# Kernel tuning notes

Measured on AMD Instinct MI355X. Metric: run time of the kernel, lower is better.

## Reference

```python
import jax, jax.numpy as jnp
import numpy as np

# 8 neighbor offsets (dy, dx) matching the torch module's kernel order:
# TL, T, TR, L, R, BL, B, BR
OFFSETS = [(-1, -1), (-1, 0), (-1, 1), (0, -1), (0, 1), (1, -1), (1, 0), (1, 1)]


def _cos_map(x):
    # x: [B, C, H, W] -> [B, 8, H-2, W-2]
    B, C, H, W = x.shape
    c = x[:, :, 1:H - 1, 1:W - 1]                       # center pixels
    xx = jnp.sum(c * c, axis=1, keepdims=True)          # [B,1,H-2,W-2]
    rxx = jax.lax.rsqrt(xx)
    maps = []
    for dy, dx in OFFSETS:
        n = x[:, :, 1 + dy:H - 1 + dy, 1 + dx:W - 1 + dx]  # shifted neighbor
        dot = jnp.sum(c * n, axis=1, keepdims=True)
        aa = jnp.sum(n * n, axis=1, keepdims=True)
        # ((x+a)^2 sum - (x^2+a^2) sum)/2 == dot; then cosine scaling
        maps.append(dot * rxx * jax.lax.rsqrt(aa))
    return jnp.concatenate(maps, axis=1)                # [B,8,H-2,W-2]


def setup_inputs() -> dict:
    key = jax.random.key(0)
    k1, k2 = jax.random.split(key)
    B, C, H, W = 16, 19, 256, 256
    preds = jax.random.normal(k1, (B, C, H, W), dtype=jnp.float32)
    soft = jax.random.normal(k2, (B, C, H, W), dtype=jnp.float32)
    return {"preds": preds, "soft": soft}


def reference(preds, soft):
    graph_s = _cos_map(preds)
    graph_t = _cos_map(soft)
    return jnp.mean((graph_s - graph_t) ** 2)
```

## Files before the change

kernel.cpp:

```cpp
#include <hip/hip_runtime.h>
#include <math.h>


constexpr int BATCH = 16;
constexpr int CH = 19;
constexpr int H = 256;
constexpr int W = 256;

constexpr int TX = 64;
constexpr int TY = 8;
constexpr int TW = TX + 2;
constexpr int THH = TY + 2;
constexpr int TILE = TW * THH;
constexpr int NTHREADS = TX * TY;

__global__ __launch_bounds__(NTHREADS)
void cosmap_mse_kernel(const float* __restrict__ preds,
                       const float* __restrict__ soft,
                       double* __restrict__ acc) {
  __shared__ float sp[TILE];
  __shared__ float ss[TILE];
  __shared__ float rnp[TILE];
  __shared__ float rns[TILE];

  const int tx = threadIdx.x;
  const int ty = threadIdx.y;
  const int tid = ty * TX + tx;
  const int b = blockIdx.z;
  const int x0 = 1 + blockIdx.x * TX;
  const int y0 = 1 + blockIdx.y * TY;

  const int idx0 = tid;
  const bool has2 = (tid + NTHREADS) < TILE;
  const int idx1 = has2 ? tid + NTHREADS : tid;

  auto goff = [&](int idx) -> int {
    int j = idx / TW;
    int i = idx - j * TW;
    int gy = y0 - 1 + j; gy = gy > H - 1 ? H - 1 : gy;
    int gx = x0 - 1 + i; gx = gx > W - 1 ? W - 1 : gx;
    return gy * W + gx;
  };
  const int off0 = goff(idx0);
  const int off1 = goff(idx1);

  const size_t base = (size_t)b * CH * H * W;
  const float* pp = preds + base;
  const float* ps = soft + base;

  float dotp[8], dots[8];
#pragma unroll
  for (int k = 0; k < 8; ++k) { dotp[k] = 0.f; dots[k] = 0.f; }
  float xxp0 = 0.f, xxs0 = 0.f, xxp1 = 0.f, xxs1 = 0.f;

  const int ci = (ty + 1) * TW + (tx + 1);

  for (int c = 0; c < CH; ++c) {
    const size_t cb = (size_t)c * (H * W);
    float vp0 = pp[cb + off0];
    float vs0 = ps[cb + off0];
    float vp1 = pp[cb + off1];
    float vs1 = ps[cb + off1];
    sp[idx0] = vp0; ss[idx0] = vs0;
    if (has2) { sp[idx1] = vp1; ss[idx1] = vs1; }
    xxp0 = fmaf(vp0, vp0, xxp0); xxs0 = fmaf(vs0, vs0, xxs0);
    xxp1 = fmaf(vp1, vp1, xxp1); xxs1 = fmaf(vs1, vs1, xxs1);
    __syncthreads();

    const float cp = sp[ci];
    const float cs = ss[ci];
    constexpr int offs[8] = {-TW - 1, -TW, -TW + 1, -1, 1, TW - 1, TW, TW + 1};
#pragma unroll
    for (int k = 0; k < 8; ++k) {
      dotp[k] = fmaf(cp, sp[ci + offs[k]], dotp[k]);
      dots[k] = fmaf(cs, ss[ci + offs[k]], dots[k]);
    }
    __syncthreads();
  }

  rnp[idx0] = 1.0f / sqrtf(xxp0);
  rns[idx0] = 1.0f / sqrtf(xxs0);
  if (has2) {
    rnp[idx1] = 1.0f / sqrtf(xxp1);
    rns[idx1] = 1.0f / sqrtf(xxs1);
  }
  __syncthreads();

  float local = 0.f;
  const int px = x0 + tx;
  const int py = y0 + ty;
  if (px < W - 1 && py < H - 1) {
    const float rp = rnp[ci];
    const float rs = rns[ci];
    constexpr int offs[8] = {-TW - 1, -TW, -TW + 1, -1, 1, TW - 1, TW, TW + 1};
#pragma unroll
    for (int k = 0; k < 8; ++k) {
      float mp = dotp[k] * rp * rnp[ci + offs[k]];
      float ms = dots[k] * rs * rns[ci + offs[k]];
      float d = mp - ms;
      local = fmaf(d, d, local);
    }
  }

#pragma unroll
  for (int o = 32; o > 0; o >>= 1) local += __shfl_down(local, o, 64);
  __shared__ float wsum[NTHREADS / 64];
  const int wid = tid >> 6;
  const int lane = tid & 63;
  if (lane == 0) wsum[wid] = local;
  __syncthreads();
  if (tid == 0) {
    float s = 0.f;
#pragma unroll
    for (int w = 0; w < NTHREADS / 64; ++w) s += wsum[w];
    atomicAdd(acc, (double)s);
  }
}

__global__ void finalize_kernel(const double* __restrict__ acc,
                                float* __restrict__ out) {
  constexpr double cnt = (double)BATCH * 8.0 * (H - 2) * (W - 2);
  out[0] = (float)(acc[0] / cnt);
}

extern "C" void kernel_launch(void* const* d_in, const int* in_sizes, int n_in,
                              void* d_out, int out_size, void* d_ws, size_t ws_size,
                              hipStream_t stream) {
  const float* preds = (const float*)d_in[0];
  const float* soft = (const float*)d_in[1];
  double* acc = (double*)d_ws;

  hipMemsetAsync(d_ws, 0, sizeof(double), stream);

  dim3 block(TX, TY);
  dim3 grid((W - 2 + TX - 1) / TX, (H - 2 + TY - 1) / TY, BATCH);
  cosmap_mse_kernel<<<grid, block, 0, stream>>>(preds, soft, acc);
  finalize_kernel<<<1, 1, 0, stream>>>(acc, (float*)d_out);
}
```

Measured before the change: 199.4 us.

## Compute two pixels per thread with float2 loads and double-buffered shared tiles

Each thread now handles two horizontally adjacent output pixels, using float2 global loads and float2 shared-memory tiles 128 pixels wide. Shared tiles are double-buffered per channel, so only one barrier per channel is needed, and the next channel's global loads are issued before the barrier as a software prefetch. The goal is fewer load instructions, fewer barriers and better reuse of neighbour values across the two pixels. In exchange it uses more registers, launches half as many blocks, and needs extra edge handling for the right border column.

Result: faster. 183.5 us (-8.0%).

```diff
diff --git a/kernel.cpp b/kernel.cpp
--- a/kernel.cpp
+++ b/kernel.cpp
@@ -2,118 +2,161 @@
 #include <math.h>
 
 
-constexpr int BATCH = 16;
-constexpr int CH = 19;
-constexpr int H = 256;
-constexpr int W = 256;
+constexpr int BATCH = 16, CH = 19, H = 256, W = 256;
+constexpr int BXT = 64, BYT = 8, NT = BXT * BYT;
+constexpr int CX = 128, CY = 8;
+constexpr int TW2 = 66;
+constexpr int TH = 10;
+constexpr int NP = TW2 * TH;
 
-constexpr int TX = 64;
-constexpr int TY = 8;
-constexpr int TW = TX + 2;
-constexpr int THH = TY + 2;
-constexpr int TILE = TW * THH;
-constexpr int NTHREADS = TX * TY;
-
-__global__ __launch_bounds__(NTHREADS)
+__global__ __launch_bounds__(NT)
 void cosmap_mse_kernel(const float* __restrict__ preds,
                        const float* __restrict__ soft,
-                       double* __restrict__ acc) {
-  __shared__ float sp[TILE];
-  __shared__ float ss[TILE];
-  __shared__ float rnp[TILE];
-  __shared__ float rns[TILE];
+                       double* __restrict__ acc_out) {
+  __shared__ float2 sp[2][NP];
+  __shared__ float2 ss[2][NP];
+  __shared__ float wsum[NT / 64];
 
-  const int tx = threadIdx.x;
-  const int ty = threadIdx.y;
-  const int tid = ty * TX + tx;
-  const int b = blockIdx.z;
-  const int x0 = 1 + blockIdx.x * TX;
-  const int y0 = 1 + blockIdx.y * TY;
+  const int tx = threadIdx.x, ty = threadIdx.y;
+  const int tid = ty * BXT + tx;
+  const int x0 = 1 + blockIdx.x * CX;
+  const int y0 = 1 + blockIdx.y * CY;
 
-  const int idx0 = tid;
-  const bool has2 = (tid + NTHREADS) < TILE;
-  const int idx1 = has2 ? tid + NTHREADS : tid;
+  const int p0 = tid;
+  const bool has2 = tid < (NP - NT);
+  const int p1 = has2 ? tid + NT : tid;
 
-  auto goff = [&](int idx) -> int {
-    int j = idx / TW;
-    int i = idx - j * TW;
+  bool ov0 = false, ov1 = false;
+  int e0, e1;
+  {
+    int j = p0 / TW2, i2 = p0 - j * TW2;
     int gy = y0 - 1 + j; gy = gy > H - 1 ? H - 1 : gy;
-    int gx = x0 - 1 + i; gx = gx > W - 1 ? W - 1 : gx;
-    return gy * W + gx;
-  };
-  const int off0 = goff(idx0);
-  const int off1 = goff(idx1);
+    int gs = x0 - 1 + 2 * i2;
+    ov0 = gs >= W - 1;
+    e0 = gy * W + (ov0 ? W - 2 : gs);
+  }
+  {
+    int j = p1 / TW2, i2 = p1 - j * TW2;
+    int gy = y0 - 1 + j; gy = gy > H - 1 ? H - 1 : gy;
+    int gs = x0 - 1 + 2 * i2;
+    ov1 = gs >= W - 1;
+    e1 = gy * W + (ov1 ? W - 2 : gs);
+  }
 
-  const size_t base = (size_t)b * CH * H * W;
-  const float* pp = preds + base;
-  const float* ps = soft + base;
+  const size_t base = (size_t)blockIdx.z * CH * H * W;
+  const float2* pp = (const float2*)(preds + base);
+  const float2* qq = (const float2*)(soft + base);
+  const int f0 = e0 >> 1, f1 = e1 >> 1;
+  constexpr int CS2 = H * W / 2;
 
-  float dotp[8], dots[8];
+  float2 vp0 = pp[f0], vq0 = qq[f0], vp1 = pp[f1], vq1 = qq[f1];
+
+  float a[8], bb[8], c[8], d[8];
 #pragma unroll
-  for (int k = 0; k < 8; ++k) { dotp[k] = 0.f; dots[k] = 0.f; }
-  float xxp0 = 0.f, xxs0 = 0.f, xxp1 = 0.f, xxs1 = 0.f;
+  for (int k = 0; k < 8; ++k) { a[k] = 0.f; bb[k] = 0.f; c[k] = 0.f; d[k] = 0.f; }
+  float2 np0 = {0.f, 0.f}, np1 = {0.f, 0.f}, nq0 = {0.f, 0.f}, nq1 = {0.f, 0.f};
 
-  const int ci = (ty + 1) * TW + (tx + 1);
+  const int r0 = ty * TW2 + tx;
 
-  for (int c = 0; c < CH; ++c) {
-    const size_t cb = (size_t)c * (H * W);
-    float vp0 = pp[cb + off0];
-    float vs0 = ps[cb + off0];
-    float vp1 = pp[cb + off1];
-    float vs1 = ps[cb + off1];
-    sp[idx0] = vp0; ss[idx0] = vs0;
-    if (has2) { sp[idx1] = vp1; ss[idx1] = vs1; }
-    xxp0 = fmaf(vp0, vp0, xxp0); xxs0 = fmaf(vs0, vs0, xxs0);
-    xxp1 = fmaf(vp1, vp1, xxp1); xxs1 = fmaf(vs1, vs1, xxs1);
-    __syncthreads();
-
-    const float cp = sp[ci];
-    const float cs = ss[ci];
-    constexpr int offs[8] = {-TW - 1, -TW, -TW + 1, -1, 1, TW - 1, TW, TW + 1};
-#pragma unroll
-    for (int k = 0; k < 8; ++k) {
-      dotp[k] = fmaf(cp, sp[ci + offs[k]], dotp[k]);
-      dots[k] = fmaf(cs, ss[ci + offs[k]], dots[k]);
+  for (int ch = 0; ch < CH; ++ch) {
+    float2* SP = sp[ch & 1];
+    float2* SS = ss[ch & 1];
+    float2 wp0 = vp0; if (ov0) wp0.x = wp0.y;
+    float2 wq0 = vq0; if (ov0) wq0.x = wq0.y;
+    float2 wp1 = vp1; if (ov1) wp1.x = wp1.y;
+    float2 wq1 = vq1; if (ov1) wq1.x = wq1.y;
+    SP[p0] = wp0; SS[p0] = wq0;
+    if (has2) { SP[p1] = wp1; SS[p1] = wq1; }
+    np0.x = fmaf(wp0.x, wp0.x, np0.x); np0.y = fmaf(wp0.y, wp0.y, np0.y);
+    nq0.x = fmaf(wq0.x, wq0.x, nq0.x); nq0.y = fmaf(wq0.y, wq0.y, nq0.y);
+    if (has2) {
+      np1.x = fmaf(wp1.x, wp1.x, np1.x); np1.y = fmaf(wp1.y, wp1.y, np1.y);
+      nq1.x = fmaf(wq1.x, wq1.x, nq1.x); nq1.y = fmaf(wq1.y, wq1.y, nq1.y);
+    }
+    if (ch + 1 < CH) {
+      const int o = (ch + 1) * CS2;
+      vp0 = pp[f0 + o]; vq0 = qq[f0 + o];
+      vp1 = pp[f1 + o]; vq1 = qq[f1 + o];
     }
     __syncthreads();
+    {
+      float2 u0 = SP[r0],           u1 = SP[r0 + 1];
+      float2 m0 = SP[r0 + TW2],     m1 = SP[r0 + TW2 + 1];
+      float2 l0 = SP[r0 + 2 * TW2], l1 = SP[r0 + 2 * TW2 + 1];
+      float c0 = m0.y, c1 = m1.x;
+      a[0] = fmaf(c0, u0.x, a[0]); a[1] = fmaf(c0, u0.y, a[1]); a[2] = fmaf(c0, u1.x, a[2]);
+      a[3] = fmaf(c0, m0.x, a[3]); a[4] = fmaf(c0, m1.x, a[4]);
+      a[5] = fmaf(c0, l0.x, a[5]); a[6] = fmaf(c0, l0.y, a[6]); a[7] = fmaf(c0, l1.x, a[7]);
+      bb[0] = fmaf(c1, u0.y, bb[0]); bb[1] = fmaf(c1, u1.x, bb[1]); bb[2] = fmaf(c1, u1.y, bb[2]);
+      bb[3] = fmaf(c1, m0.y, bb[3]); bb[4] = fmaf(c1, m1.y, bb[4]);
+      bb[5] = fmaf(c1, l0.y, bb[5]); bb[6] = fmaf(c1, l1.x, bb[6]); bb[7] = fmaf(c1, l1.y, bb[7]);
+    }
+    {
+      float2 u0 = SS[r0],           u1 = SS[r0 + 1];
+      float2 m0 = SS[r0 + TW2],     m1 = SS[r0 + TW2 + 1];
+      float2 l0 = SS[r0 + 2 * TW2], l1 = SS[r0 + 2 * TW2 + 1];
+      float c0 = m0.y, c1 = m1.x;
+      c[0] = fmaf(c0, u0.x, c[0]); c[1] = fmaf(c0, u0.y, c[1]); c[2] = fmaf(c0, u1.x, c[2]);
+      c[3] = fmaf(c0, m0.x, c[3]); c[4] = fmaf(c0, m1.x, c[4]);
+      c[5] = fmaf(c0, l0.x, c[5]); c[6] = fmaf(c0, l0.y, c[6]); c[7] = fmaf(c0, l1.x, c[7]);
+      d[0] = fmaf(c1, u0.y, d[0]); d[1] = fmaf(c1, u1.x, d[1]); d[2] = fmaf(c1, u1.y, d[2]);
+      d[3] = fmaf(c1, m0.y, d[3]); d[4] = fmaf(c1, m1.y, d[4]);
+      d[5] = fmaf(c1, l0.y, d[5]); d[6] = fmaf(c1, l1.x, d[6]); d[7] = fmaf(c1, l1.y, d[7]);
+    }
   }
 
-  rnp[idx0] = 1.0f / sqrtf(xxp0);
-  rns[idx0] = 1.0f / sqrtf(xxs0);
-  if (has2) {
-    rnp[idx1] = 1.0f / sqrtf(xxp1);
-    rns[idx1] = 1.0f / sqrtf(xxs1);
+  {
+    float2 r;
+    r.x = 1.0f / sqrtf(np0.x); r.y = 1.0f / sqrtf(np0.y); sp[1][p0] = r;
+    r.x = 1.0f / sqrtf(nq0.x); r.y = 1.0f / sqrtf(nq0.y); ss[1][p0] = r;
+    if (has2) {
+      r.x = 1.0f / sqrtf(np1.x); r.y = 1.0f / sqrtf(np1.y); sp[1][p1] = r;
+      r.x = 1.0f / sqrtf(nq1.x); r.y = 1.0f / sqrtf(nq1.y); ss[1][p1] = r;
+    }
   }
   __syncthreads();
 
   float local = 0.f;
-  const int px = x0 + tx;
-  const int py = y0 + ty;
-  if (px < W - 1 && py < H - 1) {
-    const float rp = rnp[ci];
-    const float rs = rns[ci];
-    constexpr int offs[8] = {-TW - 1, -TW, -TW + 1, -1, 1, TW - 1, TW, TW + 1};
+  {
+    const float2* RP = sp[1];
+    const float2* RS = ss[1];
+    float2 u0 = RP[r0],           u1 = RP[r0 + 1];
+    float2 m0 = RP[r0 + TW2],     m1 = RP[r0 + TW2 + 1];
+    float2 l0 = RP[r0 + 2 * TW2], l1 = RP[r0 + 2 * TW2 + 1];
+    float2 su0 = RS[r0],           su1 = RS[r0 + 1];
+    float2 sm0 = RS[r0 + TW2],     sm1 = RS[r0 + TW2 + 1];
+    float2 sl0 = RS[r0 + 2 * TW2], sl1 = RS[r0 + 2 * TW2 + 1];
+    float rc0 = m0.y, rc1 = m1.x, sc0 = sm0.y, sc1 = sm1.x;
+    float n0p[8] = {u0.x, u0.y, u1.x, m0.x, m1.x, l0.x, l0.y, l1.x};
+    float n1p[8] = {u0.y, u1.x, u1.y, m0.y, m1.y, l0.y, l1.x, l1.y};
+    float n0s[8] = {su0.x, su0.y, su1.x, sm0.x, sm1.x, sl0.x, sl0.y, sl1.x};
+    float n1s[8] = {su0.y, su1.x, su1.y, sm0.y, sm1.y, sl0.y, sl1.x, sl1.y};
+    float acc0 = 0.f, acc1 = 0.f;
 #pragma unroll
     for (int k = 0; k < 8; ++k) {
-      float mp = dotp[k] * rp * rnp[ci + offs[k]];
-      float ms = dots[k] * rs * rns[ci + offs[k]];
-      float d = mp - ms;
-      local = fmaf(d, d, local);
+      float mp = a[k] * rc0 * n0p[k];
+      float ms = c[k] * sc0 * n0s[k];
+      float dd = mp - ms;
+      acc0 = fmaf(dd, dd, acc0);
+      float mp1 = bb[k] * rc1 * n1p[k];
+      float ms1 = d[k] * sc1 * n1s[k];
+      float d1v = mp1 - ms1;
+      acc1 = fmaf(d1v, d1v, acc1);
     }
+    const int cgx = x0 + 2 * tx, cgy = y0 + ty;
+    const bool vy = cgy <= H - 2;
+    local = (vy && cgx <= W - 2 ? acc0 : 0.f) + (vy && cgx + 1 <= W - 2 ? acc1 : 0.f);
   }
 
 #pragma unroll
   for (int o = 32; o > 0; o >>= 1) local += __shfl_down(local, o, 64);
-  __shared__ float wsum[NTHREADS / 64];
-  const int wid = tid >> 6;
-  const int lane = tid & 63;
-  if (lane == 0) wsum[wid] = local;
+  if ((tid & 63) == 0) wsum[tid >> 6] = local;
   __syncthreads();
   if (tid == 0) {
     float s = 0.f;
 #pragma unroll
-    for (int w = 0; w < NTHREADS / 64; ++w) s += wsum[w];
-    atomicAdd(acc, (double)s);
+    for (int w = 0; w < NT / 64; ++w) s += wsum[w];
+    atomicAdd(acc_out, (double)s);
   }
 }
 
@@ -132,8 +175,8 @@
 
   hipMemsetAsync(d_ws, 0, sizeof(double), stream);
 
-  dim3 block(TX, TY);
-  dim3 grid((W - 2 + TX - 1) / TX, (H - 2 + TY - 1) / TY, BATCH);
+  dim3 block(BXT, BYT);
+  dim3 grid((W - 2 + CX - 1) / CX, (H - 2 + CY - 1) / CY, BATCH);
   cosmap_mse_kernel<<<grid, block, 0, stream>>>(preds, soft, acc);
   finalize_kernel<<<1, 1, 0, stream>>>(acc, (float*)d_out);
 }
```

## Replace shared-memory tiles with per-wave row processing using float4 loads and shuffles

Applied to the files above, without the earlier changes.

Each wavefront now handles one output row across the full width. Every lane loads float4 vectors from the three adjacent rows for both inputs and exchanges horizontal neighbors with lane shuffles instead of shared memory and block barriers. The next channel's loads are prefetched in registers, and each wave issues its own atomic add. This removes LDS traffic and __syncthreads, but each input row is now read three times (once per neighboring output row), and register pressure goes up.

Result: slower. 210.2 us (+5.4%).

```diff
diff --git a/kernel.cpp b/kernel.cpp
--- a/kernel.cpp
+++ b/kernel.cpp
@@ -2,119 +2,111 @@
 #include <math.h>
 
 
-constexpr int BATCH = 16;
-constexpr int CH = 19;
-constexpr int H = 256;
-constexpr int W = 256;
+constexpr int BATCH = 16, CH = 19, H = 256, W = 256;
+constexpr int HW = H * W;
+constexpr int CS4 = HW / 4;
 
-constexpr int TX = 64;
-constexpr int TY = 8;
-constexpr int TW = TX + 2;
-constexpr int THH = TY + 2;
-constexpr int TILE = TW * THH;
-constexpr int NTHREADS = TX * TY;
-
-__global__ __launch_bounds__(NTHREADS)
+__global__ __launch_bounds__(256)
 void cosmap_mse_kernel(const float* __restrict__ preds,
                        const float* __restrict__ soft,
-                       double* __restrict__ acc) {
-  __shared__ float sp[TILE];
-  __shared__ float ss[TILE];
-  __shared__ float rnp[TILE];
-  __shared__ float rns[TILE];
+                       double* __restrict__ acc_out) {
+  const int lane = threadIdx.x & 63;
+  const int wid = threadIdx.x >> 6;
+  const int y = 1 + (blockIdx.y << 2) + wid;
+  if (y > H - 2) return;
+  const size_t base = (size_t)blockIdx.z * (CH * HW);
 
-  const int tx = threadIdx.x;
-  const int ty = threadIdx.y;
-  const int tid = ty * TX + tx;
-  const int b = blockIdx.z;
-  const int x0 = 1 + blockIdx.x * TX;
-  const int y0 = 1 + blockIdx.y * TY;
+  const float4* PU = (const float4*)(preds + base + (size_t)(y - 1) * W) + lane;
+  const float4* PM = PU + (W / 4);
+  const float4* PL = PM + (W / 4);
+  const float4* SU = (const float4*)(soft + base + (size_t)(y - 1) * W) + lane;
+  const float4* SM = SU + (W / 4);
+  const float4* SL = SM + (W / 4);
 
-  const int idx0 = tid;
-  const bool has2 = (tid + NTHREADS) < TILE;
-  const int idx1 = has2 ? tid + NTHREADS : tid;
+  float dp[8][4], dq[8][4];
+  float np[3][4], nq[3][4];
+#pragma unroll
+  for (int d = 0; d < 8; ++d)
+#pragma unroll
+    for (int e = 0; e < 4; ++e) { dp[d][e] = 0.f; dq[d][e] = 0.f; }
+#pragma unroll
+  for (int r = 0; r < 3; ++r)
+#pragma unroll
+    for (int e = 0; e < 4; ++e) { np[r][e] = 0.f; nq[r][e] = 0.f; }
 
-  auto goff = [&](int idx) -> int {
-    int j = idx / TW;
-    int i = idx - j * TW;
-    int gy = y0 - 1 + j; gy = gy > H - 1 ? H - 1 : gy;
-    int gx = x0 - 1 + i; gx = gx > W - 1 ? W - 1 : gx;
-    return gy * W + gx;
-  };
-  const int off0 = goff(idx0);
-  const int off1 = goff(idx1);
-
-  const size_t base = (size_t)b * CH * H * W;
-  const float* pp = preds + base;
-  const float* ps = soft + base;
-
-  float dotp[8], dots[8];
-#pragma unroll
-  for (int k = 0; k < 8; ++k) { dotp[k] = 0.f; dots[k] = 0.f; }
-  float xxp0 = 0.f, xxs0 = 0.f, xxp1 = 0.f, xxs1 = 0.f;
-
-  const int ci = (ty + 1) * TW + (tx + 1);
+  float4 au = PU[0], am = PM[0], al = PL[0];
+  float4 bu = SU[0], bm = SM[0], bl = SL[0];
 
   for (int c = 0; c < CH; ++c) {
-    const size_t cb = (size_t)c * (H * W);
-    float vp0 = pp[cb + off0];
-    float vs0 = ps[cb + off0];
-    float vp1 = pp[cb + off1];
-    float vs1 = ps[cb + off1];
-    sp[idx0] = vp0; ss[idx0] = vs0;
-    if (has2) { sp[idx1] = vp1; ss[idx1] = vs1; }
-    xxp0 = fmaf(vp0, vp0, xxp0); xxs0 = fmaf(vs0, vs0, xxs0);
-    xxp1 = fmaf(vp1, vp1, xxp1); xxs1 = fmaf(vs1, vs1, xxs1);
-    __syncthreads();
-
-    const float cp = sp[ci];
-    const float cs = ss[ci];
-    constexpr int offs[8] = {-TW - 1, -TW, -TW + 1, -1, 1, TW - 1, TW, TW + 1};
+    const float4 cu = au, cm = am, cl = al, eu = bu, em = bm, el = bl;
+    if (c + 1 < CH) {
+      const int o = (c + 1) * CS4;
+      au = PU[o]; am = PM[o]; al = PL[o];
+      bu = SU[o]; bm = SM[o]; bl = SL[o];
+    }
+    const float wu[6] = {__shfl_up(cu.w, 1), cu.x, cu.y, cu.z, cu.w, __shfl_down(cu.x, 1)};
+    const float wm[6] = {__shfl_up(cm.w, 1), cm.x, cm.y, cm.z, cm.w, __shfl_down(cm.x, 1)};
+    const float wl[6] = {__shfl_up(cl.w, 1), cl.x, cl.y, cl.z, cl.w, __shfl_down(cl.x, 1)};
+    const float vu[6] = {__shfl_up(eu.w, 1), eu.x, eu.y, eu.z, eu.w, __shfl_down(eu.x, 1)};
+    const float vm[6] = {__shfl_up(em.w, 1), em.x, em.y, em.z, em.w, __shfl_down(em.x, 1)};
+    const float vl[6] = {__shfl_up(el.w, 1), el.x, el.y, el.z, el.w, __shfl_down(el.x, 1)};
 #pragma unroll
-    for (int k = 0; k < 8; ++k) {
-      dotp[k] = fmaf(cp, sp[ci + offs[k]], dotp[k]);
-      dots[k] = fmaf(cs, ss[ci + offs[k]], dots[k]);
+    for (int e = 0; e < 4; ++e) {
+      np[0][e] = fmaf(wu[e + 1], wu[e + 1], np[0][e]);
+      np[1][e] = fmaf(wm[e + 1], wm[e + 1], np[1][e]);
+      np[2][e] = fmaf(wl[e + 1], wl[e + 1], np[2][e]);
+      nq[0][e] = fmaf(vu[e + 1], vu[e + 1], nq[0][e]);
+      nq[1][e] = fmaf(vm[e + 1], vm[e + 1], nq[1][e]);
+      nq[2][e] = fmaf(vl[e + 1], vl[e + 1], nq[2][e]);
+      const float cp = wm[e + 1], cs = vm[e + 1];
+      dp[0][e] = fmaf(cp, wu[e],     dp[0][e]); dq[0][e] = fmaf(cs, vu[e],     dq[0][e]);
+      dp[1][e] = fmaf(cp, wu[e + 1], dp[1][e]); dq[1][e] = fmaf(cs, vu[e + 1], dq[1][e]);
+      dp[2][e] = fmaf(cp, wu[e + 2], dp[2][e]); dq[2][e] = fmaf(cs, vu[e + 2], dq[2][e]);
+      dp[3][e] = fmaf(cp, wm[e],     dp[3][e]); dq[3][e] = fmaf(cs, vm[e],     dq[3][e]);
+      dp[4][e] = fmaf(cp, wm[e + 2], dp[4][e]); dq[4][e] = fmaf(cs, vm[e + 2], dq[4][e]);
+      dp[5][e] = fmaf(cp, wl[e],     dp[5][e]); dq[5][e] = fmaf(cs, vl[e],     dq[5][e]);
+      dp[6][e] = fmaf(cp, wl[e + 1], dp[6][e]); dq[6][e] = fmaf(cs, vl[e + 1], dq[6][e]);
+      dp[7][e] = fmaf(cp, wl[e + 2], dp[7][e]); dq[7][e] = fmaf(cs, vl[e + 2], dq[7][e]);
     }
-    __syncthreads();
   }
 
-  rnp[idx0] = 1.0f / sqrtf(xxp0);
-  rns[idx0] = 1.0f / sqrtf(xxs0);
-  if (has2) {
-    rnp[idx1] = 1.0f / sqrtf(xxp1);
-    rns[idx1] = 1.0f / sqrtf(xxs1);
-  }
-  __syncthreads();
+  float rp[3][4], rq[3][4];
+#pragma unroll
+  for (int r = 0; r < 3; ++r)
+#pragma unroll
+    for (int e = 0; e < 4; ++e) {
+      rp[r][e] = 1.0f / sqrtf(np[r][e]);
+      rq[r][e] = 1.0f / sqrtf(nq[r][e]);
+    }
+
+  const float xu[6] = {__shfl_up(rp[0][3], 1), rp[0][0], rp[0][1], rp[0][2], rp[0][3], __shfl_down(rp[0][0], 1)};
+  const float xm[6] = {__shfl_up(rp[1][3], 1), rp[1][0], rp[1][1], rp[1][2], rp[1][3], __shfl_down(rp[1][0], 1)};
+  const float xl[6] = {__shfl_up(rp[2][3], 1), rp[2][0], rp[2][1], rp[2][2], rp[2][3], __shfl_down(rp[2][0], 1)};
+  const float zu[6] = {__shfl_up(rq[0][3], 1), rq[0][0], rq[0][1], rq[0][2], rq[0][3], __shfl_down(rq[0][0], 1)};
+  const float zm[6] = {__shfl_up(rq[1][3], 1), rq[1][0], rq[1][1], rq[1][2], rq[1][3], __shfl_down(rq[1][0], 1)};
+  const float zl[6] = {__shfl_up(rq[2][3], 1), rq[2][0], rq[2][1], rq[2][2], rq[2][3], __shfl_down(rq[2][0], 1)};
 
   float local = 0.f;
-  const int px = x0 + tx;
-  const int py = y0 + ty;
-  if (px < W - 1 && py < H - 1) {
-    const float rp = rnp[ci];
-    const float rs = rns[ci];
-    constexpr int offs[8] = {-TW - 1, -TW, -TW + 1, -1, 1, TW - 1, TW, TW + 1};
 #pragma unroll
-    for (int k = 0; k < 8; ++k) {
-      float mp = dotp[k] * rp * rnp[ci + offs[k]];
-      float ms = dots[k] * rs * rns[ci + offs[k]];
-      float d = mp - ms;
-      local = fmaf(d, d, local);
+  for (int e = 0; e < 4; ++e) {
+    const int x = (lane << 2) + e;
+    if (x >= 1 && x <= W - 2) {
+      const float rcp = rp[1][e], rcq = rq[1][e];
+      float mp, ms, t;
+      mp = dp[0][e] * rcp * xu[e];     ms = dq[0][e] * rcq * zu[e];     t = mp - ms; local = fmaf(t, t, local);
+      mp = dp[1][e] * rcp * xu[e + 1]; ms = dq[1][e] * rcq * zu[e + 1]; t = mp - ms; local = fmaf(t, t, local);
+      mp = dp[2][e] * rcp * xu[e + 2]; ms = dq[2][e] * rcq * zu[e + 2]; t = mp - ms; local = fmaf(t, t, local);
+      mp = dp[3][e] * rcp * xm[e];     ms = dq[3][e] * rcq * zm[e];     t = mp - ms; local = fmaf(t, t, local);
+      mp = dp[4][e] * rcp * xm[e + 2]; ms = dq[4][e] * rcq * zm[e + 2]; t = mp - ms; local = fmaf(t, t, local);
+      mp = dp[5][e] * rcp * xl[e];     ms = dq[5][e] * rcq * zl[e];     t = mp - ms; local = fmaf(t, t, local);
+      mp = dp[6][e] * rcp * xl[e + 1]; ms = dq[6][e] * rcq * zl[e + 1]; t = mp - ms; local = fmaf(t, t, local);
+      mp = dp[7][e] * rcp * xl[e + 2]; ms = dq[7][e] * rcq * zl[e + 2]; t = mp - ms; local = fmaf(t, t, local);
     }
   }
 
 #pragma unroll
   for (int o = 32; o > 0; o >>= 1) local += __shfl_down(local, o, 64);
-  __shared__ float wsum[NTHREADS / 64];
-  const int wid = tid >> 6;
-  const int lane = tid & 63;
-  if (lane == 0) wsum[wid] = local;
-  __syncthreads();
-  if (tid == 0) {
-    float s = 0.f;
-#pragma unroll
-    for (int w = 0; w < NTHREADS / 64; ++w) s += wsum[w];
-    atomicAdd(acc, (double)s);
-  }
+  if (lane == 0) atomicAdd(acc_out, (double)local);
 }
 
 __global__ void finalize_kernel(const double* __restrict__ acc,
@@ -132,8 +124,8 @@
 
   hipMemsetAsync(d_ws, 0, sizeof(double), stream);
 
-  dim3 block(TX, TY);
-  dim3 grid((W - 2 + TX - 1) / TX, (H - 2 + TY - 1) / TY, BATCH);
+  dim3 block(256);
+  dim3 grid(1, (H - 2 + 3) / 4, BATCH);
   cosmap_mse_kernel<<<grid, block, 0, stream>>>(preds, soft, acc);
   finalize_kernel<<<1, 1, 0, stream>>>(acc, (float*)d_out);
 }
```
